# Kernel optimization log

Measured on AMD Instinct MI355X. Metric: run time of the kernel, lower is better.

Reference implementation:

```python
import jax, jax.numpy as jnp
import numpy as np

N, SB, SBR, Y, C, H, NBF = 5000, 49, 19, 2, 128, 256, 512
E = 10000


def setup_inputs() -> dict:
    key = jax.random.key(0)
    ks = jax.random.split(key, 12)
    s = lambda fan_in: 1.0 / np.sqrt(fan_in)
    return {
        "x": jax.random.normal(ks[0], (N, SB, C), jnp.float32),
        "x_edge": jax.random.normal(ks[1], (E, NBF), jnp.float32),
        "edge_index": jax.random.randint(ks[2], (2, E), 0, N, jnp.int64 if jax.config.jax_enable_x64 else jnp.int32),
        "wigner": jax.random.normal(ks[3], (E * Y, SBR, SB), jnp.float32) * s(SB),
        "wigner_inv": jax.random.normal(ks[4], (E, SB, SBR), jnp.float32) * s(SBR),
        "w_dist": jax.random.normal(ks[5], (NBF, H), jnp.float32) * s(NBF),
        "b_dist": jnp.zeros((H,), jnp.float32),
        "w_proj": jax.random.normal(ks[6], (2 * SBR * C, H), jnp.float32) * s(2 * SBR * C),
        "b_proj": jnp.zeros((H,), jnp.float32),
        "w_edge": jax.random.normal(ks[7], (H, H), jnp.float32) * s(H),
        "b_edge": jnp.zeros((H,), jnp.float32),
        "w_out": jax.random.normal(ks[8], (H, SBR * C), jnp.float32) * s(H),
        "b_out": jnp.zeros((SBR * C,), jnp.float32),
    }


def reference(x, x_edge, edge_index, wigner, wigner_inv,
              w_dist, b_dist, w_proj, b_proj, w_edge, b_edge, w_out, b_out):
    act = jax.nn.silu
    # distance embedding gate: [E, H]
    x_edge = act(x_edge @ w_dist + b_dist)
    # edge gathers: [E, SB, C]
    x_source = x[edge_index[0]]
    x_target = x[edge_index[1]]

    def rotate(v):
        # repeat each edge for Y y-rotations, then rotate with per-(edge,rot) Wigner matrix
        v = jnp.broadcast_to(v[:, None], (E, Y, SB, C)).reshape(E * Y, SB, C)
        r = jnp.einsum("ers,esc->erc", wigner, v)  # [E*Y, SBR, C]
        return r.reshape(E * Y, SBR * C)

    x_message = jnp.concatenate([rotate(x_source), rotate(x_target)], axis=1)  # [E*Y, 2*SBR*C]
    x_message = act(x_message @ w_proj + b_proj)  # [E*Y, H]
    # gate by distance embedding (broadcast over y rotations)
    x_message = (x_message.reshape(E, Y, H) * x_edge[:, None, :]).reshape(E * Y, H)
    x_message = act(x_message @ w_edge + b_edge)
    x_message = act(x_message @ w_out + b_out)  # [E*Y, SBR*C]
    # CombineYRotations: average over the Y rotated copies
    x_message = x_message.reshape(E, Y, SBR, C).mean(axis=1)  # [E, SBR, C]
    # RotateInv: back to full spherical basis per edge
    return jnp.einsum("ebs,esc->ebc", wigner_inv, x_message)  # [E, SB, C]
```

## Files before the change

### kernel.cpp

```cpp
#include <hip/hip_runtime.h>

#define E_N   10000
#define SB_N  49
#define SBR_N 19
#define C_N   128
#define H_N   256
#define NBF_N 512
#define KPROJ 4864
#define NOUT  2432
#define BPAD  56

typedef _Float16 f16x8 __attribute__((ext_vector_type(8)));
typedef _Float16 f16x4 __attribute__((ext_vector_type(4)));
typedef _Float16 f16x2 __attribute__((ext_vector_type(2)));
typedef float    f32x4 __attribute__((ext_vector_type(4)));

__device__ __forceinline__ float silu_f(float v) { return v / (1.0f + __expf(-v)); }

__device__ __forceinline__ float dot2f(f16x2 a, f16x2 b, float c) {
#if defined(__has_builtin)
#if __has_builtin(__builtin_amdgcn_fdot2)
    return __builtin_amdgcn_fdot2(a, b, c, false);
#else
    return c + (float)a[0] * (float)b[0] + (float)a[1] * (float)b[1];
#endif
#else
    return c + (float)a[0] * (float)b[0] + (float)a[1] * (float)b[1];
#endif
}

#define GLOBAL_PTR(p) ((const __attribute__((address_space(1))) void*)(p))
#define LDS_PTR(p)    ((__attribute__((address_space(3))) void*)(p))

__launch_bounds__(256)
__global__ void transpose_to_f16(const float* __restrict__ in, _Float16* __restrict__ out,
                                 int K, int N)
{
    __shared__ float tile[32][33];
    const int k0 = blockIdx.x * 32;
    const int n0 = blockIdx.y * 32;
    const int tx = threadIdx.x & 31;
    const int ty = threadIdx.x >> 5;
    #pragma unroll
    for (int i = ty; i < 32; i += 8)
        if (k0 + i < K && n0 + tx < N)
            tile[i][tx] = in[(size_t)(k0 + i) * N + (n0 + tx)];
    __syncthreads();
    #pragma unroll
    for (int i = ty; i < 32; i += 8)
        if (n0 + i < N && k0 + tx < K)
            out[(size_t)(n0 + i) * K + (k0 + tx)] = (_Float16)tile[tx][i];
}

__launch_bounds__(256)
__global__ void cvt_to_f16(const float* __restrict__ in, _Float16* __restrict__ out, int n4)
{
    int i = blockIdx.x * blockDim.x + threadIdx.x;
    const int stride = gridDim.x * blockDim.x;
    for (; i < n4; i += stride) {
        const float4 v = ((const float4*)in)[i];
        f16x4 o; o[0] = (_Float16)v.x; o[1] = (_Float16)v.y; o[2] = (_Float16)v.z; o[3] = (_Float16)v.w;
        ((f16x4*)out)[i] = o;
    }
}

__launch_bounds__(256)
__global__ void prep_xt(const float* __restrict__ x, _Float16* __restrict__ xt)
{
    __shared__ float xs[SB_N * C_N];
    __shared__ _Float16 xl[C_N * BPAD];
    const int n = blockIdx.x;
    const int tid = threadIdx.x;
    for (int t = tid; t < (SB_N * C_N) / 4; t += 256)
        ((float4*)xs)[t] = ((const float4*)(x + (size_t)n * (SB_N * C_N)))[t];
    __syncthreads();
    for (int t = tid; t < C_N * (BPAD / 2); t += 256) {
        const int c = t & 127;
        const int j = t >> 7;
        const int b0 = 2 * j, b1 = 2 * j + 1;
        f16x2 p;
        p[0] = (b0 < SB_N) ? (_Float16)xs[b0 * C_N + c] : (_Float16)0.f;
        p[1] = (b1 < SB_N) ? (_Float16)xs[b1 * C_N + c] : (_Float16)0.f;
        ((f16x2*)xl)[c * (BPAD / 2) + j] = p;
    }
    __syncthreads();
    _Float16* dst = xt + (size_t)n * (C_N * BPAD);
    for (int t = tid; t < (C_N * BPAD) / 4; t += 256)
        ((f16x4*)dst)[t] = ((const f16x4*)xl)[t];
}

template<int GATED>
__launch_bounds__(256, 2)
__global__ void gemm_f16(const _Float16* __restrict__ A, int lda,
                         const _Float16* __restrict__ BT,
                         const float* __restrict__ bias,
                         const _Float16* __restrict__ gate,
                         _Float16* __restrict__ C,
                         int M, int N, int K, int i0)
{
    __shared__ __align__(16) _Float16 As[4][128][8];
    __shared__ __align__(16) _Float16 Bs[4][128][8];
    const int tid  = threadIdx.x;
    const int lane = tid & 63;
    const int w    = tid >> 6;
    const int wr   = w >> 1;
    const int wc   = w & 1;
    const int n0   = blockIdx.x * 128;
    const int m0   = blockIdx.y * 128;

    const int r01 = tid & 127;
    const int ks0 = tid >> 7;
    const int ks1 = ks0 + 2;
    const _Float16* a0 = A  + (size_t)(m0 + r01) * lda + ks0 * 8;
    const _Float16* a1 = A  + (size_t)(m0 + r01) * lda + ks1 * 8;
    const _Float16* b0 = BT + (size_t)(n0 + r01) * K   + ks0 * 8;
    const _Float16* b1 = BT + (size_t)(n0 + r01) * K   + ks1 * 8;
    _Float16* sA0 = &As[0][0][0] + (size_t)tid * 8;
    _Float16* sA1 = sA0 + 2048;
    _Float16* sB0 = &Bs[0][0][0] + (size_t)tid * 8;
    _Float16* sB1 = sB0 + 2048;

    const int frow = lane & 15;
    const int fks  = lane >> 4;
    const _Float16* fA = &As[fks][wr * 64 + frow][0];
    const _Float16* fB = &Bs[fks][wc * 64 + frow][0];

    f32x4 acc[4][4] = {};

    for (int k0 = 0; k0 < K; k0 += 32) {
        __builtin_amdgcn_global_load_lds(GLOBAL_PTR(a0 + k0), LDS_PTR(sA0), 16, 0, 0);
        __builtin_amdgcn_global_load_lds(GLOBAL_PTR(a1 + k0), LDS_PTR(sA1), 16, 0, 0);
        __builtin_amdgcn_global_load_lds(GLOBAL_PTR(b0 + k0), LDS_PTR(sB0), 16, 0, 0);
        __builtin_amdgcn_global_load_lds(GLOBAL_PTR(b1 + k0), LDS_PTR(sB1), 16, 0, 0);
        __syncthreads();
        f16x8 af[4], bf[4];
        #pragma unroll
        for (int m = 0; m < 4; ++m) af[m] = *(const f16x8*)(fA + m * 16 * 8);
        #pragma unroll
        for (int n = 0; n < 4; ++n) bf[n] = *(const f16x8*)(fB + n * 16 * 8);
        #pragma unroll
        for (int m = 0; m < 4; ++m)
            #pragma unroll
            for (int n = 0; n < 4; ++n)
                acc[m][n] = __builtin_amdgcn_mfma_f32_16x16x32_f16(af[m], bf[n], acc[m][n], 0, 0, 0);
        __syncthreads();
    }

    #pragma unroll
    for (int m = 0; m < 4; ++m) {
        #pragma unroll
        for (int n = 0; n < 4; ++n) {
            const int gn = n0 + wc * 64 + n * 16 + (lane & 15);
            #pragma unroll
            for (int r = 0; r < 4; ++r) {
                const int gm = m0 + wr * 64 + m * 16 + (lane >> 4) * 4 + r;
                if (gm < M) {
                    float v = acc[m][n][r] + bias[gn];
                    v = silu_f(v);
                    if (GATED) v *= (float)gate[(size_t)((i0 + gm) >> 1) * H_N + gn];
                    C[(size_t)gm * N + gn] = (_Float16)v;
                }
            }
        }
    }
}

__launch_bounds__(256)
__global__ void rotate_v2(const _Float16* __restrict__ xt, const float* __restrict__ wigner,
                          const int* __restrict__ eidx, _Float16* __restrict__ rot, int e0)
{
    __shared__ __align__(16) _Float16 xs_t[2][C_N * BPAD];
    __shared__ __align__(16) _Float16 wg[2][SBR_N * BPAD];
    const int tid = threadIdx.x;
    const int e = e0 + blockIdx.x;
    const int node0 = eidx[0 * E_N + e];
    const int node1 = eidx[1 * E_N + e];

    const f16x8* s0 = (const f16x8*)(xt + (size_t)node0 * (C_N * BPAD));
    const f16x8* s1 = (const f16x8*)(xt + (size_t)node1 * (C_N * BPAD));
    for (int t = tid; t < (C_N * BPAD) / 8; t += 256) {
        *(f16x8*)&xs_t[0][t * 8] = s0[t];
        *(f16x8*)&xs_t[1][t * 8] = s1[t];
    }
    for (int t = tid; t < 2 * SBR_N * SB_N; t += 256) {
        const int y = t / (SBR_N * SB_N);
        const int sb = t - y * (SBR_N * SB_N);
        const int s = sb / SB_N, b = sb - s * SB_N;
        wg[y][s * BPAD + b] = (_Float16)wigner[((size_t)(2 * e) + y) * (SBR_N * SB_N) + sb];
    }
    for (int t = tid; t < 2 * SBR_N * (BPAD - SB_N); t += 256) {
        const int y = t / (SBR_N * (BPAD - SB_N));
        const int r = t - y * (SBR_N * (BPAD - SB_N));
        const int s = r / (BPAD - SB_N), j = r - s * (BPAD - SB_N);
        wg[y][s * BPAD + SB_N + j] = (_Float16)0.f;
    }
    __syncthreads();

    const int c = tid & 127;
    const int part = tid >> 7;

    f16x2 xc[BPAD / 2];
    const f16x2* xr = (const f16x2*)&xs_t[part][c * BPAD];
    #pragma unroll
    for (int j = 0; j < BPAD / 2; ++j) xc[j] = xr[j];

    const size_t rowbase = 2 * (size_t)blockIdx.x;
    #pragma unroll
    for (int y = 0; y < 2; ++y) {
        _Float16* orow = rot + (rowbase + y) * KPROJ + part * NOUT + c;
        for (int s = 0; s < SBR_N; ++s) {
            const f16x2* wr = (const f16x2*)&wg[y][s * BPAD];
            float acc = 0.f;
            #pragma unroll
            for (int j = 0; j < BPAD / 2; ++j)
                acc = dot2f(xc[j], wr[j], acc);
            orow[s * C_N] = (_Float16)acc;
        }
    }
}

__launch_bounds__(128)
__global__ void combine_kernel(const _Float16* __restrict__ h3, const float* __restrict__ wigner_inv,
                               float* __restrict__ out, int e0)
{
    __shared__ float ms[SBR_N * C_N];
    __shared__ float wv[SB_N * SBR_N];
    const int eb = blockIdx.x;
    const int e = e0 + eb;
    const int c = threadIdx.x;

    #pragma unroll
    for (int s = 0; s < SBR_N; ++s) {
        const float a = (float)h3[(size_t)(2 * eb) * NOUT + s * C_N + c];
        const float b = (float)h3[(size_t)(2 * eb + 1) * NOUT + s * C_N + c];
        ms[s * C_N + c] = 0.5f * (a + b);
    }
    for (int t = c; t < SB_N * SBR_N; t += 128)
        wv[t] = wigner_inv[(size_t)e * (SB_N * SBR_N) + t];
    __syncthreads();

    for (int b = 0; b < SB_N; ++b) {
        float acc = 0.f;
        #pragma unroll
        for (int s = 0; s < SBR_N; ++s)
            acc += wv[b * SBR_N + s] * ms[s * C_N + c];
        out[(size_t)e * (SB_N * C_N) + b * C_N + c] = acc;
    }
}

extern "C" void kernel_launch(void* const* d_in, const int* in_sizes, int n_in,
                              void* d_out, int out_size, void* d_ws, size_t ws_size,
                              hipStream_t stream)
{
    const float* x          = (const float*)d_in[0];
    const float* x_edge     = (const float*)d_in[1];
    const int*   eidx       = (const int*)d_in[2];
    const float* wigner     = (const float*)d_in[3];
    const float* wigner_inv = (const float*)d_in[4];
    const float* w_dist     = (const float*)d_in[5];
    const float* b_dist     = (const float*)d_in[6];
    const float* w_proj     = (const float*)d_in[7];
    const float* b_proj     = (const float*)d_in[8];
    const float* w_edge     = (const float*)d_in[9];
    const float* b_edge     = (const float*)d_in[10];
    const float* w_out      = (const float*)d_in[11];
    const float* b_out      = (const float*)d_in[12];
    float* out = (float*)d_out;

    char* wsp = (char*)d_ws;
    auto alloc = [&](size_t bytes) -> char* {
        char* p = wsp;
        wsp += (bytes + 255) & ~(size_t)255;
        return p;
    };
    const int XE_ROWS = 10112;
    _Float16* gate = (_Float16*)alloc((size_t)E_N * H_N * sizeof(_Float16));
    _Float16* wTd  = (_Float16*)alloc((size_t)H_N * NBF_N * sizeof(_Float16));
    _Float16* wTp  = (_Float16*)alloc((size_t)H_N * KPROJ * sizeof(_Float16));
    _Float16* wTe  = (_Float16*)alloc((size_t)H_N * H_N * sizeof(_Float16));
    _Float16* wTo  = (_Float16*)alloc((size_t)NOUT * H_N * sizeof(_Float16));
    _Float16* xeh  = (_Float16*)alloc((size_t)XE_ROWS * NBF_N * sizeof(_Float16));
    _Float16* xt   = (_Float16*)alloc((size_t)5000 * C_N * BPAD * sizeof(_Float16));

    const size_t used = (size_t)(wsp - (char*)d_ws);
    const size_t avail = ws_size > used ? ws_size - used : 0;
    const size_t per_row = (size_t)(KPROJ + H_N + H_N) * sizeof(_Float16);
    long cimax = (long)(avail / per_row) & ~127L;
    if (cimax > 20096) cimax = 20096;
    if (cimax < 128) cimax = 128;

    _Float16* rot = (_Float16*)alloc((size_t)cimax * KPROJ * sizeof(_Float16));
    _Float16* h1  = (_Float16*)alloc((size_t)cimax * H_N * sizeof(_Float16));
    _Float16* h2  = (_Float16*)alloc((size_t)cimax * H_N * sizeof(_Float16));

    transpose_to_f16<<<dim3(NBF_N / 32, H_N / 32), 256, 0, stream>>>(w_dist, wTd, NBF_N, H_N);
    transpose_to_f16<<<dim3(KPROJ / 32, H_N / 32), 256, 0, stream>>>(w_proj, wTp, KPROJ, H_N);
    transpose_to_f16<<<dim3(H_N / 32, H_N / 32), 256, 0, stream>>>(w_edge, wTe, H_N, H_N);
    transpose_to_f16<<<dim3(H_N / 32, NOUT / 32), 256, 0, stream>>>(w_out, wTo, H_N, NOUT);
    cvt_to_f16<<<dim3(1024), 256, 0, stream>>>(x_edge, xeh, (E_N * NBF_N) / 4);
    prep_xt<<<dim3(5000), 256, 0, stream>>>(x, xt);

    gemm_f16<0><<<dim3(H_N / 128, XE_ROWS / 128), 256, 0, stream>>>(
        xeh, NBF_N, wTd, b_dist, nullptr, gate, E_N, H_N, NBF_N, 0);

    for (long i0 = 0; i0 < 2L * E_N; i0 += cimax) {
        long ci = 2L * E_N - i0;
        if (ci > cimax) ci = cimax;
        const unsigned cb = (unsigned)((ci + 127) / 128);

        rotate_v2<<<dim3((unsigned)(ci / 2)), 256, 0, stream>>>(
            xt, wigner, eidx, rot, (int)(i0 / 2));

        gemm_f16<1><<<dim3(H_N / 128, cb), 256, 0, stream>>>(
            rot, KPROJ, wTp, b_proj, gate, h1, (int)ci, H_N, KPROJ, (int)i0);

        gemm_f16<0><<<dim3(H_N / 128, cb), 256, 0, stream>>>(
            h1, H_N, wTe, b_edge, nullptr, h2, (int)ci, H_N, H_N, 0);

        gemm_f16<0><<<dim3(NOUT / 128, cb), 256, 0, stream>>>(
            h2, H_N, wTo, b_out, nullptr, rot, (int)ci, NOUT, H_N, 0);

        combine_kernel<<<dim3((unsigned)(ci / 2)), 128, 0, stream>>>(
            rot, wigner_inv, out, (int)(i0 / 2));
    }
}
```

Before: 1.037 ms.

## Shrink GEMM tiles to 64x64 with double-buffered LDS and XCD-aware block remap

The f16 MFMA GEMM moves from 128x128 tiles with a 32-wide K step to 64x64 tiles with a 64-wide K step. LDS is now double-buffered, so the next K slice loads while the current one is multiplied, and the kernel runs on a 1D grid whose block index is remapped per XCD. The 128x128 tiling gave only a few hundred blocks for the N=256 GEMMs, which leaves many CUs idle. The new tiling produces roughly four times as many blocks and targets higher occupancy, at the cost of less operand reuse per tile. The main loop assumes K/64 is even, which holds for the current K values.

```diff
diff --git a/kernel.cpp b/kernel.cpp
--- a/kernel.cpp
+++ b/kernel.cpp
@@ -90,7 +90,7 @@
 }
 
 template<int GATED>
-__launch_bounds__(256, 2)
+__launch_bounds__(256, 4)
 __global__ void gemm_f16(const _Float16* __restrict__ A, int lda,
                          const _Float16* __restrict__ BT,
                          const float* __restrict__ bias,
@@ -98,64 +98,91 @@
                          _Float16* __restrict__ C,
                          int M, int N, int K, int i0)
 {
-    __shared__ __align__(16) _Float16 As[4][128][8];
-    __shared__ __align__(16) _Float16 Bs[4][128][8];
+    __shared__ __align__(16) _Float16 As[2][8][64][8];
+    __shared__ __align__(16) _Float16 Bs[2][8][64][8];
     const int tid  = threadIdx.x;
     const int lane = tid & 63;
     const int w    = tid >> 6;
     const int wr   = w >> 1;
     const int wc   = w & 1;
-    const int n0   = blockIdx.x * 128;
-    const int m0   = blockIdx.y * 128;
-
-    const int r01 = tid & 127;
-    const int ks0 = tid >> 7;
-    const int ks1 = ks0 + 2;
-    const _Float16* a0 = A  + (size_t)(m0 + r01) * lda + ks0 * 8;
-    const _Float16* a1 = A  + (size_t)(m0 + r01) * lda + ks1 * 8;
-    const _Float16* b0 = BT + (size_t)(n0 + r01) * K   + ks0 * 8;
-    const _Float16* b1 = BT + (size_t)(n0 + r01) * K   + ks1 * 8;
-    _Float16* sA0 = &As[0][0][0] + (size_t)tid * 8;
-    _Float16* sA1 = sA0 + 2048;
-    _Float16* sB0 = &Bs[0][0][0] + (size_t)tid * 8;
-    _Float16* sB1 = sB0 + 2048;
+
+    const unsigned nwg = gridDim.x;
+    const unsigned q = nwg >> 3, r = nwg & 7;
+    const unsigned xcd = blockIdx.x & 7, lo = blockIdx.x >> 3;
+    const unsigned g = (xcd < r ? xcd * (q + 1) : r * (q + 1) + (xcd - r) * q) + lo;
+    const int nbn = N >> 6;
+    const int n0 = (int)(g % (unsigned)nbn) * 64;
+    const int m0 = (int)(g / (unsigned)nbn) * 64;
+
+    const int rs = tid & 63;
+    const int ks = tid >> 6;
+    const _Float16* ag = A  + (size_t)(m0 + rs) * lda + ks * 8;
+    const _Float16* bg = BT + (size_t)(n0 + rs) * K   + ks * 8;
+    _Float16* sa0 = &As[0][0][0][0] + tid * 8;
+    _Float16* sa1 = &As[1][0][0][0] + tid * 8;
+    _Float16* sb0 = &Bs[0][0][0][0] + tid * 8;
+    _Float16* sb1 = &Bs[1][0][0][0] + tid * 8;
 
     const int frow = lane & 15;
     const int fks  = lane >> 4;
-    const _Float16* fA = &As[fks][wr * 64 + frow][0];
-    const _Float16* fB = &Bs[fks][wc * 64 + frow][0];
-
-    f32x4 acc[4][4] = {};
-
-    for (int k0 = 0; k0 < K; k0 += 32) {
-        __builtin_amdgcn_global_load_lds(GLOBAL_PTR(a0 + k0), LDS_PTR(sA0), 16, 0, 0);
-        __builtin_amdgcn_global_load_lds(GLOBAL_PTR(a1 + k0), LDS_PTR(sA1), 16, 0, 0);
-        __builtin_amdgcn_global_load_lds(GLOBAL_PTR(b0 + k0), LDS_PTR(sB0), 16, 0, 0);
-        __builtin_amdgcn_global_load_lds(GLOBAL_PTR(b1 + k0), LDS_PTR(sB1), 16, 0, 0);
+    const _Float16* fA0 = &As[0][fks][wr * 32 + frow][0];
+    const _Float16* fA1 = &As[1][fks][wr * 32 + frow][0];
+    const _Float16* fB0 = &Bs[0][fks][wc * 32 + frow][0];
+    const _Float16* fB1 = &Bs[1][fks][wc * 32 + frow][0];
+
+    f32x4 acc[2][2] = {};
+
+#define STAGE(SA, SB, KOFF) do {                                                          \
+    __builtin_amdgcn_global_load_lds(GLOBAL_PTR(ag + (KOFF)),      LDS_PTR(SA),        16, 0, 0); \
+    __builtin_amdgcn_global_load_lds(GLOBAL_PTR(ag + (KOFF) + 32), LDS_PTR(SA + 2048), 16, 0, 0); \
+    __builtin_amdgcn_global_load_lds(GLOBAL_PTR(bg + (KOFF)),      LDS_PTR(SB),        16, 0, 0); \
+    __builtin_amdgcn_global_load_lds(GLOBAL_PTR(bg + (KOFF) + 32), LDS_PTR(SB + 2048), 16, 0, 0); \
+} while (0)
+
+#define COMPUTE(FA, FB) do {                                                   \
+    const f16x8 a0m0 = *(const f16x8*)(FA);                                    \
+    const f16x8 a0m1 = *(const f16x8*)(FA + 128);                              \
+    const f16x8 a1m0 = *(const f16x8*)(FA + 2048);                             \
+    const f16x8 a1m1 = *(const f16x8*)(FA + 2048 + 128);                       \
+    const f16x8 b0n0 = *(const f16x8*)(FB);                                    \
+    const f16x8 b0n1 = *(const f16x8*)(FB + 128);                              \
+    const f16x8 b1n0 = *(const f16x8*)(FB + 2048);                             \
+    const f16x8 b1n1 = *(const f16x8*)(FB + 2048 + 128);                       \
+    acc[0][0] = __builtin_amdgcn_mfma_f32_16x16x32_f16(a0m0, b0n0, acc[0][0], 0, 0, 0); \
+    acc[0][1] = __builtin_amdgcn_mfma_f32_16x16x32_f16(a0m0, b0n1, acc[0][1], 0, 0, 0); \
+    acc[1][0] = __builtin_amdgcn_mfma_f32_16x16x32_f16(a0m1, b0n0, acc[1][0], 0, 0, 0); \
+    acc[1][1] = __builtin_amdgcn_mfma_f32_16x16x32_f16(a0m1, b0n1, acc[1][1], 0, 0, 0); \
+    acc[0][0] = __builtin_amdgcn_mfma_f32_16x16x32_f16(a1m0, b1n0, acc[0][0], 0, 0, 0); \
+    acc[0][1] = __builtin_amdgcn_mfma_f32_16x16x32_f16(a1m0, b1n1, acc[0][1], 0, 0, 0); \
+    acc[1][0] = __builtin_amdgcn_mfma_f32_16x16x32_f16(a1m1, b1n0, acc[1][0], 0, 0, 0); \
+    acc[1][1] = __builtin_amdgcn_mfma_f32_16x16x32_f16(a1m1, b1n1, acc[1][1], 0, 0, 0); \
+} while (0)
+
+    const int nt = K >> 6;
+    STAGE(sa0, sb0, 0);
+    __syncthreads();
+    int koff = 64;
+    for (int t = 0; t + 2 <= nt; t += 2) {
+        STAGE(sa1, sb1, koff); koff += 64;
+        COMPUTE(fA0, fB0);
         __syncthreads();
-        f16x8 af[4], bf[4];
+        if (t + 2 < nt) { STAGE(sa0, sb0, koff); koff += 64; }
+        COMPUTE(fA1, fB1);
+        __syncthreads();
+    }
+#undef STAGE
+#undef COMPUTE
+
+    #pragma unroll
+    for (int m = 0; m < 2; ++m) {
         #pragma unroll
-        for (int m = 0; m < 4; ++m) af[m] = *(const f16x8*)(fA + m * 16 * 8);
-        #pragma unroll
-        for (int n = 0; n < 4; ++n) bf[n] = *(const f16x8*)(fB + n * 16 * 8);
-        #pragma unroll
-        for (int m = 0; m < 4; ++m)
+        for (int n = 0; n < 2; ++n) {
+            const int gn = n0 + wc * 32 + n * 16 + (lane & 15);
             #pragma unroll
-            for (int n = 0; n < 4; ++n)
-                acc[m][n] = __builtin_amdgcn_mfma_f32_16x16x32_f16(af[m], bf[n], acc[m][n], 0, 0, 0);
-        __syncthreads();
-    }
-
-    #pragma unroll
-    for (int m = 0; m < 4; ++m) {
-        #pragma unroll
-        for (int n = 0; n < 4; ++n) {
-            const int gn = n0 + wc * 64 + n * 16 + (lane & 15);
-            #pragma unroll
-            for (int r = 0; r < 4; ++r) {
-                const int gm = m0 + wr * 64 + m * 16 + (lane >> 4) * 4 + r;
+            for (int rr = 0; rr < 4; ++rr) {
+                const int gm = m0 + wr * 32 + m * 16 + (lane >> 4) * 4 + rr;
                 if (gm < M) {
-                    float v = acc[m][n][r] + bias[gn];
+                    float v = acc[m][n][rr] + bias[gn];
                     v = silu_f(v);
                     if (GATED) v *= (float)gate[(size_t)((i0 + gm) >> 1) * H_N + gn];
                     C[(size_t)gm * N + gn] = (_Float16)v;
@@ -190,8 +217,8 @@
     }
     for (int t = tid; t < 2 * SBR_N * (BPAD - SB_N); t += 256) {
         const int y = t / (SBR_N * (BPAD - SB_N));
-        const int r = t - y * (SBR_N * (BPAD - SB_N));
-        const int s = r / (BPAD - SB_N), j = r - s * (BPAD - SB_N);
+        const int rr = t - y * (SBR_N * (BPAD - SB_N));
+        const int s = rr / (BPAD - SB_N), j = rr - s * (BPAD - SB_N);
         wg[y][s * BPAD + SB_N + j] = (_Float16)0.f;
     }
     __syncthreads();
@@ -209,11 +236,11 @@
     for (int y = 0; y < 2; ++y) {
         _Float16* orow = rot + (rowbase + y) * KPROJ + part * NOUT + c;
         for (int s = 0; s < SBR_N; ++s) {
-            const f16x2* wr = (const f16x2*)&wg[y][s * BPAD];
+            const f16x2* wrp = (const f16x2*)&wg[y][s * BPAD];
             float acc = 0.f;
             #pragma unroll
             for (int j = 0; j < BPAD / 2; ++j)
-                acc = dot2f(xc[j], wr[j], acc);
+                acc = dot2f(xc[j], wrp[j], acc);
             orow[s * C_N] = (_Float16)acc;
         }
     }
@@ -300,24 +327,24 @@
     cvt_to_f16<<<dim3(1024), 256, 0, stream>>>(x_edge, xeh, (E_N * NBF_N) / 4);
     prep_xt<<<dim3(5000), 256, 0, stream>>>(x, xt);
 
-    gemm_f16<0><<<dim3(H_N / 128, XE_ROWS / 128), 256, 0, stream>>>(
+    gemm_f16<0><<<dim3((H_N / 64) * (XE_ROWS / 64)), 256, 0, stream>>>(
         xeh, NBF_N, wTd, b_dist, nullptr, gate, E_N, H_N, NBF_N, 0);
 
     for (long i0 = 0; i0 < 2L * E_N; i0 += cimax) {
         long ci = 2L * E_N - i0;
         if (ci > cimax) ci = cimax;
-        const unsigned cb = (unsigned)((ci + 127) / 128);
+        const unsigned mb = (unsigned)((ci + 63) / 64);
 
         rotate_v2<<<dim3((unsigned)(ci / 2)), 256, 0, stream>>>(
             xt, wigner, eidx, rot, (int)(i0 / 2));
 
-        gemm_f16<1><<<dim3(H_N / 128, cb), 256, 0, stream>>>(
+        gemm_f16<1><<<dim3((H_N / 64) * mb), 256, 0, stream>>>(
             rot, KPROJ, wTp, b_proj, gate, h1, (int)ci, H_N, KPROJ, (int)i0);
 
-        gemm_f16<0><<<dim3(H_N / 128, cb), 256, 0, stream>>>(
+        gemm_f16<0><<<dim3((H_N / 64) * mb), 256, 0, stream>>>(
             h1, H_N, wTe, b_edge, nullptr, h2, (int)ci, H_N, H_N, 0);
 
-        gemm_f16<0><<<dim3(NOUT / 128, cb), 256, 0, stream>>>(
+        gemm_f16<0><<<dim3((NOUT / 64) * mb), 256, 0, stream>>>(
             h2, H_N, wTo, b_out, nullptr, rot, (int)ci, NOUT, H_N, 0);
 
         combine_kernel<<<dim3((unsigned)(ci / 2)), 128, 0, stream>>>(
```

Measured after the change: 1.082 ms. 4.3% more time.

## Split-K the projection GEMM with a fused reduce, bias, SiLU and gate kernel

Applied to the files above, without the earlier changes.

The K=4864 projection GEMM, which previously launched only 2×cb tiles, is now split into four K chunks over a third grid dimension. Each chunk writes fp32 partials to a new workspace buffer. A separate grid-stride kernel then sums the partials and applies bias, SiLU and the distance gate to produce h1. This is meant to fill more CUs and shorten each block's serial K loop, at the cost of extra fp32 partial traffic and one more launch per chunk. The workspace sizing is adjusted for the partials, and a few local variables in rotate_v2 are renamed.

```diff
diff --git a/kernel.cpp b/kernel.cpp
--- a/kernel.cpp
+++ b/kernel.cpp
@@ -9,6 +9,8 @@
 #define KPROJ 4864
 #define NOUT  2432
 #define BPAD  56
+#define KSPLIT 4
+#define KCH   (KPROJ / KSPLIT)
 
 typedef _Float16 f16x8 __attribute__((ext_vector_type(8)));
 typedef _Float16 f16x4 __attribute__((ext_vector_type(4)));
@@ -165,6 +167,104 @@
     }
 }
 
+__launch_bounds__(256, 2)
+__global__ void gemm_f16_splitk(const _Float16* __restrict__ A, int lda,
+                                const _Float16* __restrict__ BT,
+                                float* __restrict__ partial, size_t pstride,
+                                int N)
+{
+    __shared__ __align__(16) _Float16 As[4][128][8];
+    __shared__ __align__(16) _Float16 Bs[4][128][8];
+    const int tid  = threadIdx.x;
+    const int lane = tid & 63;
+    const int w    = tid >> 6;
+    const int wr   = w >> 1;
+    const int wc   = w & 1;
+    const int n0   = blockIdx.x * 128;
+    const int m0   = blockIdx.y * 128;
+    const int kspl = blockIdx.z;
+
+    const int r01 = tid & 127;
+    const int ks0 = tid >> 7;
+    const int ks1 = ks0 + 2;
+    const _Float16* a0 = A  + (size_t)(m0 + r01) * lda + kspl * KCH + ks0 * 8;
+    const _Float16* a1 = A  + (size_t)(m0 + r01) * lda + kspl * KCH + ks1 * 8;
+    const _Float16* b0 = BT + (size_t)(n0 + r01) * KPROJ + kspl * KCH + ks0 * 8;
+    const _Float16* b1 = BT + (size_t)(n0 + r01) * KPROJ + kspl * KCH + ks1 * 8;
+    _Float16* sA0 = &As[0][0][0] + (size_t)tid * 8;
+    _Float16* sA1 = sA0 + 2048;
+    _Float16* sB0 = &Bs[0][0][0] + (size_t)tid * 8;
+    _Float16* sB1 = sB0 + 2048;
+
+    const int frow = lane & 15;
+    const int fks  = lane >> 4;
+    const _Float16* fA = &As[fks][wr * 64 + frow][0];
+    const _Float16* fB = &Bs[fks][wc * 64 + frow][0];
+
+    f32x4 acc[4][4] = {};
+
+    for (int k0 = 0; k0 < KCH; k0 += 32) {
+        __builtin_amdgcn_global_load_lds(GLOBAL_PTR(a0 + k0), LDS_PTR(sA0), 16, 0, 0);
+        __builtin_amdgcn_global_load_lds(GLOBAL_PTR(a1 + k0), LDS_PTR(sA1), 16, 0, 0);
+        __builtin_amdgcn_global_load_lds(GLOBAL_PTR(b0 + k0), LDS_PTR(sB0), 16, 0, 0);
+        __builtin_amdgcn_global_load_lds(GLOBAL_PTR(b1 + k0), LDS_PTR(sB1), 16, 0, 0);
+        __syncthreads();
+        f16x8 af[4], bf[4];
+        #pragma unroll
+        for (int m = 0; m < 4; ++m) af[m] = *(const f16x8*)(fA + m * 16 * 8);
+        #pragma unroll
+        for (int n = 0; n < 4; ++n) bf[n] = *(const f16x8*)(fB + n * 16 * 8);
+        #pragma unroll
+        for (int m = 0; m < 4; ++m)
+            #pragma unroll
+            for (int n = 0; n < 4; ++n)
+                acc[m][n] = __builtin_amdgcn_mfma_f32_16x16x32_f16(af[m], bf[n], acc[m][n], 0, 0, 0);
+        __syncthreads();
+    }
+
+    float* pout = partial + (size_t)kspl * pstride;
+    #pragma unroll
+    for (int m = 0; m < 4; ++m) {
+        #pragma unroll
+        for (int n = 0; n < 4; ++n) {
+            const int gn = n0 + wc * 64 + n * 16 + (lane & 15);
+            #pragma unroll
+            for (int r = 0; r < 4; ++r) {
+                const int gm = m0 + wr * 64 + m * 16 + (lane >> 4) * 4 + r;
+                pout[(size_t)gm * N + gn] = acc[m][n][r];
+            }
+        }
+    }
+}
+
+__launch_bounds__(256)
+__global__ void reduce_silu_gate(const float* __restrict__ partial, size_t pstride,
+                                 const float* __restrict__ bias,
+                                 const _Float16* __restrict__ gate,
+                                 _Float16* __restrict__ h1, int ci, int i0)
+{
+    const int total = ci * (H_N / 4);
+    const int gstride = gridDim.x * blockDim.x;
+    for (int idx = blockIdx.x * blockDim.x + threadIdx.x; idx < total; idx += gstride) {
+        const int m = idx >> 6;
+        const int n = (idx & 63) * 4;
+        const size_t off = (size_t)m * H_N + n;
+        const float4 p0 = *(const float4*)(partial + 0 * pstride + off);
+        const float4 p1 = *(const float4*)(partial + 1 * pstride + off);
+        const float4 p2 = *(const float4*)(partial + 2 * pstride + off);
+        const float4 p3 = *(const float4*)(partial + 3 * pstride + off);
+        const float4 bi = *(const float4*)(bias + n);
+        const f16x4 g = *(const f16x4*)(gate + (size_t)((i0 + m) >> 1) * H_N + n);
+        f16x4 o;
+        float v;
+        v = p0.x + p1.x + p2.x + p3.x + bi.x; v = silu_f(v) * (float)g[0]; o[0] = (_Float16)v;
+        v = p0.y + p1.y + p2.y + p3.y + bi.y; v = silu_f(v) * (float)g[1]; o[1] = (_Float16)v;
+        v = p0.z + p1.z + p2.z + p3.z + bi.z; v = silu_f(v) * (float)g[2]; o[2] = (_Float16)v;
+        v = p0.w + p1.w + p2.w + p3.w + bi.w; v = silu_f(v) * (float)g[3]; o[3] = (_Float16)v;
+        *(f16x4*)(h1 + off) = o;
+    }
+}
+
 __launch_bounds__(256)
 __global__ void rotate_v2(const _Float16* __restrict__ xt, const float* __restrict__ wigner,
                           const int* __restrict__ eidx, _Float16* __restrict__ rot, int e0)
@@ -190,8 +290,8 @@
     }
     for (int t = tid; t < 2 * SBR_N * (BPAD - SB_N); t += 256) {
         const int y = t / (SBR_N * (BPAD - SB_N));
-        const int r = t - y * (SBR_N * (BPAD - SB_N));
-        const int s = r / (BPAD - SB_N), j = r - s * (BPAD - SB_N);
+        const int rr = t - y * (SBR_N * (BPAD - SB_N));
+        const int s = rr / (BPAD - SB_N), j = rr - s * (BPAD - SB_N);
         wg[y][s * BPAD + SB_N + j] = (_Float16)0.f;
     }
     __syncthreads();
@@ -209,11 +309,11 @@
     for (int y = 0; y < 2; ++y) {
         _Float16* orow = rot + (rowbase + y) * KPROJ + part * NOUT + c;
         for (int s = 0; s < SBR_N; ++s) {
-            const f16x2* wr = (const f16x2*)&wg[y][s * BPAD];
+            const f16x2* wrp = (const f16x2*)&wg[y][s * BPAD];
             float acc = 0.f;
             #pragma unroll
             for (int j = 0; j < BPAD / 2; ++j)
-                acc = dot2f(xc[j], wr[j], acc);
+                acc = dot2f(xc[j], wrp[j], acc);
             orow[s * C_N] = (_Float16)acc;
         }
     }
@@ -284,14 +384,17 @@
 
     const size_t used = (size_t)(wsp - (char*)d_ws);
     const size_t avail = ws_size > used ? ws_size - used : 0;
-    const size_t per_row = (size_t)(KPROJ + H_N + H_N) * sizeof(_Float16);
+    const size_t per_row = (size_t)(KPROJ + H_N + H_N) * sizeof(_Float16)
+                         + (size_t)KSPLIT * H_N * sizeof(float);
     long cimax = (long)(avail / per_row) & ~127L;
     if (cimax > 20096) cimax = 20096;
     if (cimax < 128) cimax = 128;
 
-    _Float16* rot = (_Float16*)alloc((size_t)cimax * KPROJ * sizeof(_Float16));
-    _Float16* h1  = (_Float16*)alloc((size_t)cimax * H_N * sizeof(_Float16));
-    _Float16* h2  = (_Float16*)alloc((size_t)cimax * H_N * sizeof(_Float16));
+    _Float16* rot  = (_Float16*)alloc((size_t)cimax * KPROJ * sizeof(_Float16));
+    _Float16* h1   = (_Float16*)alloc((size_t)cimax * H_N * sizeof(_Float16));
+    _Float16* h2   = (_Float16*)alloc((size_t)cimax * H_N * sizeof(_Float16));
+    float*    part = (float*)alloc((size_t)KSPLIT * cimax * H_N * sizeof(float));
+    const size_t pstride = (size_t)cimax * H_N;
 
     transpose_to_f16<<<dim3(NBF_N / 32, H_N / 32), 256, 0, stream>>>(w_dist, wTd, NBF_N, H_N);
     transpose_to_f16<<<dim3(KPROJ / 32, H_N / 32), 256, 0, stream>>>(w_proj, wTp, KPROJ, H_N);
@@ -311,8 +414,16 @@
         rotate_v2<<<dim3((unsigned)(ci / 2)), 256, 0, stream>>>(
             xt, wigner, eidx, rot, (int)(i0 / 2));
 
-        gemm_f16<1><<<dim3(H_N / 128, cb), 256, 0, stream>>>(
-            rot, KPROJ, wTp, b_proj, gate, h1, (int)ci, H_N, KPROJ, (int)i0);
+        gemm_f16_splitk<<<dim3(H_N / 128, cb, KSPLIT), 256, 0, stream>>>(
+            rot, KPROJ, wTp, part, pstride, H_N);
+
+        {
+            const int total = (int)ci * (H_N / 4);
+            unsigned rb = (unsigned)((total + 255) / 256);
+            if (rb > 2048) rb = 2048;
+            reduce_silu_gate<<<dim3(rb), 256, 0, stream>>>(
+                part, pstride, b_proj, gate, h1, (int)ci, (int)i0);
+        }
 
         gemm_f16<0><<<dim3(H_N / 128, cb), 256, 0, stream>>>(
             h1, H_N, wTe, b_edge, nullptr, h2, (int)ci, H_N, H_N, 0);
```

Result: faster. 995.7 us (-4.0%).
